# Optimization experiments

Measured on AMD Instinct MI355X. Metric: run time of the kernel, lower is better.

Reference implementation:

```python
import jax, jax.numpy as jnp
import numpy as np

D_MODEL, N_STATE, L_MAX, BATCH = 512, 64, 2048, 8


def _make_dplr_hippo(n):
    # HiPPO-LegS -> NPLR -> DPLR (Annotated-S4 construction)
    p0 = np.sqrt(1.0 + 2.0 * np.arange(n))
    A = p0[:, None] * p0[None, :]
    A = -(np.tril(A) - np.diag(np.arange(n)))
    p = np.sqrt(np.arange(n) + 0.5)
    S = A + p[:, None] * p[None, :]          # normal part (skew-symmetric + const diag)
    lam_re = np.mean(np.diagonal(S)) * np.ones(n)
    lam_im, V = np.linalg.eigh(S * (-1j))
    p_rot = V.conj().T @ p
    return (lam_re.astype(np.float32), lam_im.astype(np.float32),
            p_rot.real.astype(np.float32), p_rot.imag.astype(np.float32))


def setup_inputs() -> dict:
    key = jax.random.key(0)
    k = jax.random.split(key, 8)
    lam_re, lam_im, p_re, p_im = _make_dplr_hippo(N_STATE)
    dt_min, dt_max = 1e-3, 1e-1
    log_step = (jax.random.uniform(k[0], (D_MODEL,))
                * (np.log(dt_max) - np.log(dt_min)) + np.log(dt_min)).astype(jnp.float32)
    s = 0.5 ** 0.5
    B_re = jax.random.normal(k[1], (D_MODEL, N_STATE), dtype=jnp.float32) * s
    B_im = jax.random.normal(k[2], (D_MODEL, N_STATE), dtype=jnp.float32) * s
    Ct_re = jax.random.normal(k[3], (D_MODEL, N_STATE), dtype=jnp.float32) * s
    Ct_im = jax.random.normal(k[4], (D_MODEL, N_STATE), dtype=jnp.float32) * s
    D = jnp.ones((D_MODEL,), jnp.float32)
    lim = 1.0 / np.sqrt(D_MODEL)
    W = jax.random.uniform(k[5], (D_MODEL, D_MODEL), minval=-lim, maxval=lim, dtype=jnp.float32)
    b = jax.random.uniform(k[6], (D_MODEL,), minval=-lim, maxval=lim, dtype=jnp.float32)
    u = jax.random.normal(k[7], (BATCH, L_MAX, D_MODEL), dtype=jnp.float32)
    return dict(u=u,
                lam_re=jnp.asarray(lam_re), lam_im=jnp.asarray(lam_im),
                p_re=jnp.asarray(p_re), p_im=jnp.asarray(p_im),
                B_re=B_re, B_im=B_im, Ct_re=Ct_re, Ct_im=Ct_im,
                log_step=log_step, D=D, W=W, b=b,
                ln_w=jnp.ones((D_MODEL,), jnp.float32),
                ln_b=jnp.zeros((D_MODEL,), jnp.float32))


def _s4_kernel(lam, p, Bc, Ct, step, L):
    # lam, p: (n,) complex; Bc, Ct: (H, n) complex; step: (H,)
    omega = jnp.exp((-2j * jnp.pi) * (jnp.arange(L) / L))          # (L,) roots of unity
    g = (2.0 / step[:, None]) * ((1.0 - omega) / (1.0 + omega))    # (H, L) bilinear transform
    c = 2.0 / (1.0 + omega)                                        # (L,)
    cauchy = 1.0 / (g[:, :, None] - lam)                           # (H, L, n)
    a0, a1 = Ct.conj(), jnp.conj(p)[None, :]
    b0, b1 = Bc, p[None, :]
    k00 = jnp.einsum('hn,hln->hl', a0 * b0, cauchy)
    k01 = jnp.einsum('hn,hln->hl', a0 * b1, cauchy)
    k10 = jnp.einsum('hn,hln->hl', a1 * b0, cauchy)
    k11 = jnp.einsum('hn,hln->hl', a1 * b1, cauchy)
    at_roots = c * (k00 - k01 * (1.0 / (1.0 + k11)) * k10)         # generating fn at roots
    return jnp.fft.ifft(at_roots, n=L, axis=-1).real               # (H, L) real SSM kernel


def reference(u, lam_re, lam_im, p_re, p_im, B_re, B_im, Ct_re, Ct_im,
              log_step, D, W, b, ln_w, ln_b):
    L = u.shape[1]
    lam = lam_re + 1j * lam_im
    p = p_re + 1j * p_im
    Bc = B_re + 1j * B_im
    Ct = Ct_re + 1j * Ct_im
    K = _s4_kernel(lam, p, Bc, Ct, jnp.exp(log_step), L)           # (H, L)
    # causal (non-circular) convolution via zero-padded FFT
    nfft = 2 * L
    Kf = jnp.fft.rfft(K, n=nfft, axis=-1)                          # (H, L+1)
    Uf = jnp.fft.rfft(u, n=nfft, axis=1)                           # (B, L+1, H)
    y = jnp.fft.irfft(Uf * Kf.T[None], n=nfft, axis=1)[:, :L]      # (B, L, H)
    y = y + D * u                                                  # skip connection
    z = jax.nn.gelu(y, approximate=False)                          # GELU (dropout p=0)
    z = jnp.einsum('blh,oh->blo', z, W) + b                        # Linear(d_model, d_model)
    r = z + u                                                      # residual
    mean = r.mean(-1, keepdims=True)
    var = r.var(-1, keepdims=True)
    return (r - mean) / jnp.sqrt(var + 1e-5) * ln_w + ln_b         # LayerNorm
```

## Files before the change

kernel.cpp:

```cpp
#include <hip/hip_runtime.h>
#include <hip/hip_bf16.h>
#include <math.h>

#define PI_F 3.14159265358979f

typedef __attribute__((ext_vector_type(8))) short bf16x8;
typedef __attribute__((ext_vector_type(4))) float f32x4;
typedef __attribute__((ext_vector_type(2))) float f32x2;

#define DM 512
#define LSEQ 2048
#define NB 8
#define NFFT 4096
#define MTOK (NB*LSEQ)

__device__ __forceinline__ float frcp(float x) { return __builtin_amdgcn_rcpf(x); }

__device__ __forceinline__ float gelu_fast(float y) {
  float t = 0.79788456f * (y + 0.044715f * y * y * y);
  float e = __expf(2.0f * t);
  float th = 1.0f - 2.0f * frcp(e + 1.0f);
  return 0.5f * y * (1.0f + th);
}

__device__ __forceinline__ int PD(int i) { return i + (i >> 5); }
#define LDSN 4224

template<bool INV>
__device__ __forceinline__ void dft8(const float xr[8], const float xi[8],
                                     float yr[8], float yi[8]) {
  const float C = 0.70710678118654752f;
  float t0r=xr[0]+xr[4], t0i=xi[0]+xi[4];
  float t1r=xr[0]-xr[4], t1i=xi[0]-xi[4];
  float t2r=xr[2]+xr[6], t2i=xi[2]+xi[6];
  float t3r=xr[2]-xr[6], t3i=xi[2]-xi[6];
  float it3r = INV ? -t3i : t3i;
  float it3i = INV ?  t3r : -t3r;
  float E0r=t0r+t2r, E0i=t0i+t2i;
  float E2r=t0r-t2r, E2i=t0i-t2i;
  float E1r=t1r+it3r, E1i=t1i+it3i;
  float E3r=t1r-it3r, E3i=t1i-it3i;
  float u0r=xr[1]+xr[5], u0i=xi[1]+xi[5];
  float u1r=xr[1]-xr[5], u1i=xi[1]-xi[5];
  float u2r=xr[3]+xr[7], u2i=xi[3]+xi[7];
  float u3r=xr[3]-xr[7], u3i=xi[3]-xi[7];
  float iu3r = INV ? -u3i : u3i;
  float iu3i = INV ?  u3r : -u3r;
  float O0r=u0r+u2r, O0i=u0i+u2i;
  float O2r=u0r-u2r, O2i=u0i-u2i;
  float O1r=u1r+iu3r, O1i=u1i+iu3i;
  float O3r=u1r-iu3r, O3i=u1i-iu3i;
  float w1r = INV ? C*(O1r-O1i) : C*(O1r+O1i);
  float w1i = INV ? C*(O1r+O1i) : C*(O1i-O1r);
  float w2r = INV ? -O2i : O2i;
  float w2i = INV ?  O2r : -O2r;
  float w3r = INV ? -C*(O3r+O3i) : C*(O3i-O3r);
  float w3i = INV ?  C*(O3r-O3i) : -C*(O3r+O3i);
  yr[0]=E0r+O0r; yi[0]=E0i+O0i;
  yr[4]=E0r-O0r; yi[4]=E0i-O0i;
  yr[1]=E1r+w1r; yi[1]=E1i+w1i;
  yr[5]=E1r-w1r; yi[5]=E1i-w1i;
  yr[2]=E2r+w2r; yi[2]=E2i+w2i;
  yr[6]=E2r-w2r; yi[6]=E2i-w2i;
  yr[3]=E3r+w3r; yi[3]=E3i+w3i;
  yr[7]=E3r-w3r; yi[7]=E3i-w3i;
}

template<bool INV>
__device__ __forceinline__ void dft16(const float xr[16], const float xi[16],
                                      float yr[16], float yi[16]) {
  float exr[8], exi[8], oxr[8], oxi[8];
  #pragma unroll
  for (int m = 0; m < 8; ++m) {
    exr[m]=xr[2*m];   exi[m]=xi[2*m];
    oxr[m]=xr[2*m+1]; oxi[m]=xi[2*m+1];
  }
  float er[8], ei[8], orr[8], oii[8];
  dft8<INV>(exr, exi, er, ei);
  dft8<INV>(oxr, oxi, orr, oii);
  const float KC = 0.92387953251128675f;
  const float KS = 0.38268343236508977f;
  const float KH = 0.70710678118654752f;
  float tr, ti;
  yr[0]=er[0]+orr[0]; yi[0]=ei[0]+oii[0];
  yr[8]=er[0]-orr[0]; yi[8]=ei[0]-oii[0];
  { float a=KC, b=INV?KS:-KS;
    tr=orr[1]*a-oii[1]*b; ti=orr[1]*b+oii[1]*a;
    yr[1]=er[1]+tr; yi[1]=ei[1]+ti; yr[9]=er[1]-tr; yi[9]=ei[1]-ti; }
  { float a=KH, b=INV?KH:-KH;
    tr=orr[2]*a-oii[2]*b; ti=orr[2]*b+oii[2]*a;
    yr[2]=er[2]+tr; yi[2]=ei[2]+ti; yr[10]=er[2]-tr; yi[10]=ei[2]-ti; }
  { float a=KS, b=INV?KC:-KC;
    tr=orr[3]*a-oii[3]*b; ti=orr[3]*b+oii[3]*a;
    yr[3]=er[3]+tr; yi[3]=ei[3]+ti; yr[11]=er[3]-tr; yi[11]=ei[3]-ti; }
  { if (INV) { tr=-oii[4]; ti= orr[4]; } else { tr= oii[4]; ti=-orr[4]; }
    yr[4]=er[4]+tr; yi[4]=ei[4]+ti; yr[12]=er[4]-tr; yi[12]=ei[4]-ti; }
  { float a=-KS, b=INV?KC:-KC;
    tr=orr[5]*a-oii[5]*b; ti=orr[5]*b+oii[5]*a;
    yr[5]=er[5]+tr; yi[5]=ei[5]+ti; yr[13]=er[5]-tr; yi[13]=ei[5]-ti; }
  { float a=-KH, b=INV?KH:-KH;
    tr=orr[6]*a-oii[6]*b; ti=orr[6]*b+oii[6]*a;
    yr[6]=er[6]+tr; yi[6]=ei[6]+ti; yr[14]=er[6]-tr; yi[14]=ei[6]-ti; }
  { float a=-KC, b=INV?KS:-KS;
    tr=orr[7]*a-oii[7]*b; ti=orr[7]*b+oii[7]*a;
    yr[7]=er[7]+tr; yi[7]=ei[7]+ti; yr[15]=er[7]-tr; yi[15]=ei[7]-ti; }
}

template<bool INV, int NSLOG, int NBF>
__device__ __forceinline__ void r16s(float* sr, float* si, int tid,
                                     float c1, float s1f) {
  float yr[16], yi[16];
  bool act = (NBF >= 256) || (tid < NBF);
  __syncthreads();
  if (act) {
    float xr[16], xi[16];
    #pragma unroll
    for (int m = 0; m < 16; ++m) {
      int ix = PD(tid + m * NBF);
      xr[m] = sr[ix]; xi[m] = si[ix];
    }
    if (NSLOG > 0) {
      float s1 = INV ? -s1f : s1f;
      float wr = c1, wi = s1;
      #pragma unroll
      for (int m = 1; m < 16; ++m) {
        float tr = xr[m]*wr - xi[m]*wi;
        float ti = xr[m]*wi + xi[m]*wr;
        xr[m] = tr; xi[m] = ti;
        float nr = wr*c1 - wi*s1;
        float ni = wr*s1 + wi*c1;
        wr = nr; wi = ni;
      }
    }
    dft16<INV>(xr, xi, yr, yi);
  }
  __syncthreads();
  if (act) {
    int r = tid & ((1 << NSLOG) - 1);
    int q = tid >> NSLOG;
    int base = (q << (NSLOG + 4)) + r;
    #pragma unroll
    for (int p = 0; p < 16; ++p) {
      int ix = PD(base + (p << NSLOG));
      sr[ix] = yr[p]; si[ix] = yi[p];
    }
  }
}

__device__ __forceinline__ void r16s_zfirst(float* sr, float* si, int tid) {
  const float KC = 0.92387953251128675f;
  const float KS = 0.38268343236508977f;
  const float KH = 0.70710678118654752f;
  float xr[8], xi[8];
  __syncthreads();
  #pragma unroll
  for (int m = 0; m < 8; ++m) {
    int ix = PD(tid + m * 256);
    xr[m] = sr[ix]; xi[m] = si[ix];
  }
  float er[8], ei[8];
  dft8<false>(xr, xi, er, ei);
  float tr[8], ti[8];
  tr[0] = xr[0];                      ti[0] = xi[0];
  tr[1] =  xr[1]*KC + xi[1]*KS;       ti[1] =  xi[1]*KC - xr[1]*KS;
  tr[2] = (xr[2] + xi[2])*KH;         ti[2] = (xi[2] - xr[2])*KH;
  tr[3] =  xr[3]*KS + xi[3]*KC;       ti[3] =  xi[3]*KS - xr[3]*KC;
  tr[4] =  xi[4];                     ti[4] = -xr[4];
  tr[5] = -xr[5]*KS + xi[5]*KC;       ti[5] = -xi[5]*KS - xr[5]*KC;
  tr[6] = (xi[6] - xr[6])*KH;         ti[6] = -(xr[6] + xi[6])*KH;
  tr[7] = -xr[7]*KC + xi[7]*KS;       ti[7] = -xi[7]*KC - xr[7]*KS;
  float odr[8], odi[8];
  dft8<false>(tr, ti, odr, odi);
  __syncthreads();
  int base = tid << 4;
  #pragma unroll
  for (int j = 0; j < 8; ++j) {
    int ie = PD(base + 2*j), io = PD(base + 2*j + 1);
    sr[ie] = er[j];  si[ie] = ei[j];
    sr[io] = odr[j]; si[io] = odi[j];
  }
}

template<bool INV, int NSLOG, int NBF>
__device__ __forceinline__ void r8s(float* sr, float* si, int tid,
                                    float c1, float s1f) {
  float yr[8], yi[8];
  bool act = (NBF >= 256) || (tid < NBF);
  __syncthreads();
  if (act) {
    float xr[8], xi[8];
    #pragma unroll
    for (int m = 0; m < 8; ++m) {
      int ix = PD(tid + m * NBF);
      xr[m] = sr[ix]; xi[m] = si[ix];
    }
    if (NSLOG > 0) {
      float s1 = INV ? -s1f : s1f;
      float wr = c1, wi = s1;
      #pragma unroll
      for (int m = 1; m < 8; ++m) {
        float tr = xr[m]*wr - xi[m]*wi;
        float ti = xr[m]*wi + xi[m]*wr;
        xr[m] = tr; xi[m] = ti;
        float nr = wr*c1 - wi*s1;
        float ni = wr*s1 + wi*c1;
        wr = nr; wi = ni;
      }
    }
    dft8<INV>(xr, xi, yr, yi);
  }
  __syncthreads();
  if (act) {
    int r = tid & ((1 << NSLOG) - 1);
    int q = tid >> NSLOG;
    int base = (q << (NSLOG + 3)) + r;
    #pragma unroll
    for (int p = 0; p < 8; ++p) {
      int ix = PD(base + (p << NSLOG));
      sr[ix] = yr[p]; si[ix] = yi[p];
    }
  }
}

template<bool INV>
__device__ __forceinline__ void fft4096(float* sr, float* si, int tid,
                                        float cA, float sA, float cB, float sB) {
  r16s<INV, 0, 256>(sr, si, tid, 1.f, 0.f);
  r16s<INV, 4, 256>(sr, si, tid, cA, sA);
  r16s<INV, 8, 256>(sr, si, tid, cB, sB);
  __syncthreads();
}

__device__ __forceinline__ void fft4096z(float* sr, float* si, int tid,
                                         float cA, float sA, float cB, float sB) {
  r16s_zfirst(sr, si, tid);
  r16s<false, 4, 256>(sr, si, tid, cA, sA);
  r16s<false, 8, 256>(sr, si, tid, cB, sB);
  __syncthreads();
}

template<bool INV>
__device__ __forceinline__ void fft2048(float* sr, float* si, int tid,
                                        float cA, float sA, float cB, float sB) {
  r8s <INV, 0, 256>(sr, si, tid, 1.f, 0.f);
  r16s<INV, 3, 128>(sr, si, tid, cA, sA);
  r16s<INV, 7, 128>(sr, si, tid, cB, sB);
  __syncthreads();
}

__global__ __launch_bounds__(256) void k_prep(
    const float* __restrict__ lam_re, const float* __restrict__ lam_im,
    const float* __restrict__ p_re,   const float* __restrict__ p_im,
    const float* __restrict__ B_re,   const float* __restrict__ B_im,
    const float* __restrict__ Ct_re,  const float* __restrict__ Ct_im,
    float* __restrict__ wtab, float4* __restrict__ otab) {
  int bidx = blockIdx.x;
  if (bidx < 128) {
    int idx = bidx * 256 + threadIdx.x;
    int n = idx & 63;
    float br = B_re[idx],  bi = B_im[idx];
    float cr = Ct_re[idx], ci = Ct_im[idx];
    float pr = p_re[n],    pi = p_im[n];
    float* w = wtab + (size_t)idx * 12;
    w[0] = cr*br + ci*bi;   w[1] = cr*bi - ci*br;
    w[2] = cr*pr + ci*pi;   w[3] = cr*pi - ci*pr;
    w[4] = pr*br + pi*bi;   w[5] = pr*bi - pi*br;
    w[6] = pr*pr + pi*pi;   w[7] = lam_re[n];
    w[8] = lam_im[n];       w[9] = 0.f; w[10] = 0.f; w[11] = 0.f;
  } else {
    int l = (bidx - 128) * 256 + threadIdx.x;
    float omi, omr;
    sincosf(-2.0f * PI_F * (float)l / (float)LSEQ, &omi, &omr);
    float a = 1.0f + omr;
    float iv = frcp(a*a + omi*omi);
    float4 o;
    o.x = 2.0f * a * iv;
    o.y = -2.0f * omi * iv;
    o.z = (1.0f - omr*omr - omi*omi) * iv;
    o.w = (-2.0f * omi) * iv;
    otab[l] = o;
  }
}

__global__ __launch_bounds__(256) void k_mega(
    const float* __restrict__ wtab, const float4* __restrict__ otab,
    const float* __restrict__ log_step, float2* __restrict__ atr,
    const float* __restrict__ u, float* __restrict__ ut,
    const float* __restrict__ W, __hip_bfloat16* __restrict__ Wb) {
  __shared__ float tsh[32][33];
  int bidx = blockIdx.x;
  int tid = threadIdx.x;
  int x = tid & 31, y0 = tid >> 5;

  float ur[4][4];
  #pragma unroll
  for (int t = 0; t < 4; ++t) {
    int id = bidx*4 + t;
    int lx = id & 63, hy = (id >> 6) & 15, b = id >> 10;
    int l0 = lx*32, h0 = hy*32;
    #pragma unroll
    for (int i = 0; i < 4; ++i) {
      int y = y0 + i*8;
      ur[t][i] = u[((size_t)b*LSEQ + l0 + y)*DM + h0 + x];
    }
  }
  bool doW = bidx < 1024;
  int wi = bidx*256 + tid;
  float wv = doW ? W[wi] : 0.0f;

  {
    int h = bidx >> 2;
    int l0 = ((bidx & 3) << 8) + tid;
    int l1 = l0 + 1024;
    float tos = 2.0f * expf(-log_step[h]);
    float4 o0 = otab[l0];
    float4 o1 = otab[l1];
    float cr0 = o0.x, ci0 = o0.y, cr1 = o1.x, ci1 = o1.y;
    f32x2 gr, gi;
    gr.x = tos * o0.z;  gr.y = tos * o1.z;
    gi.x = tos * o0.w;  gi.y = tos * o1.w;
    f32x2 K00r={0.f,0.f},K00i={0.f,0.f},K01r={0.f,0.f},K01i={0.f,0.f},
          K10r={0.f,0.f},K10i={0.f,0.f},K11r={0.f,0.f},K11i={0.f,0.f};
    const float4* wq = (const float4*)(wtab + (size_t)h * 64 * 12);
    #pragma unroll 8
    for (int n = 0; n < 64; ++n) {
      float4 wa = wq[n*3+0];
      float4 wb = wq[n*3+1];
      float  lim = wq[n*3+2].x;
      f32x2 dr = gr - wb.w;
      f32x2 di = gi - lim;
      f32x2 den = dr*dr + di*di;
      float ip = frcp(den.x * den.y);
      f32x2 inv; inv.x = den.y * ip; inv.y = den.x * ip;
      f32x2 car = dr*inv, cai = -di*inv;
      K00r += wa.x*car - wa.y*cai;  K00i += wa.x*cai + wa.y*car;
      K01r += wa.z*car - wa.w*cai;  K01i += wa.z*cai + wa.w*car;
      K10r += wb.x*car - wb.y*cai;  K10i += wb.x*cai + wb.y*car;
      K11r += wb.z*car;             K11i += wb.z*cai;
    }
    {
      float tr = K01r.x*K10r.x - K01i.x*K10i.x, ti = K01r.x*K10i.x + K01i.x*K10r.x;
      float d1r = 1.0f + K11r.x, d1i = K11i.x;
      float invd1 = frcp(d1r*d1r + d1i*d1i);
      float t2r = (tr*d1r + ti*d1i) * invd1;
      float t2i = (ti*d1r - tr*d1i) * invd1;
      float numr = K00r.x - t2r, numi = K00i.x - t2i;
      atr[(size_t)h * LSEQ + l0] = make_float2(cr0*numr - ci0*numi, cr0*numi + ci0*numr);
    }
    {
      float tr = K01r.y*K10r.y - K01i.y*K10i.y, ti = K01r.y*K10i.y + K01i.y*K10r.y;
      float d1r = 1.0f + K11r.y, d1i = K11i.y;
      float invd1 = frcp(d1r*d1r + d1i*d1i);
      float t2r = (tr*d1r + ti*d1i) * invd1;
      float t2i = (ti*d1r - tr*d1i) * invd1;
      float numr = K00r.y - t2r, numi = K00i.y - t2i;
      atr[(size_t)h * LSEQ + l1] = make_float2(cr1*numr - ci1*numi, cr1*numi + ci1*numr);
    }
  }

  if (doW) Wb[wi] = __float2bfloat16(wv);
  #pragma unroll
  for (int t = 0; t < 4; ++t) {
    int id = bidx*4 + t;
    int lx = id & 63, hy = (id >> 6) & 15, b = id >> 10;
    int l0 = lx*32, h0 = hy*32;
    __syncthreads();
    #pragma unroll
    for (int i = 0; i < 4; ++i)
      tsh[y0 + i*8][x] = ur[t][i];
    __syncthreads();
    #pragma unroll
    for (int i = 0; i < 4; ++i) {
      int y = y0 + i*8;
      ut[((size_t)b*DM + h0 + y)*LSEQ + l0 + x] = tsh[x][y];
    }
  }
}

__global__ __launch_bounds__(256, 4) void k_fftK(const float2* __restrict__ atr,
                                                 float2* __restrict__ Kf) {
  __shared__ float sr[LDSN], si[LDSN];
  int h = blockIdx.x, tid = threadIdx.x;
  float c2a, s2a, c2b, s2b, c4a, s4a, c4b, s4b;
  { int r = tid & 7;   __sincosf(-2.f*PI_F*(float)r/128.f,  &s2a, &c2a); }
  { int r = tid & 127; __sincosf(-2.f*PI_F*(float)r/2048.f, &s2b, &c2b); }
  { int r = tid & 15;  __sincosf(-2.f*PI_F*(float)r/256.f,  &s4a, &c4a); }
  { int r = tid;       __sincosf(-2.f*PI_F*(float)r/4096.f, &s4b, &c4b); }
  const float2* ap = atr + (size_t)h * LSEQ;
  #pragma unroll
  for (int i = 0; i < 8; ++i) {
    int l = tid + i*256;
    float2 v = ap[l];
    sr[PD(l)] = v.x; si[PD(l)] = v.y;
  }
  fft2048<true>(sr, si, tid, c2a, s2a, c2b, s2b);
  #pragma unroll
  for (int i = 0; i < 8; ++i) {
    int m = tid + i*256;
    float v = sr[PD(m)] * (1.0f / (float)LSEQ);
    sr[PD(m)] = v;
    si[PD(m)] = 0.0f;
  }
  fft4096z(sr, si, tid, c4a, s4a, c4b, s4b);
  float2* ko = Kf + (size_t)h * NFFT;
  #pragma unroll
  for (int i = 0; i < 16; ++i) {
    int f = tid + i*256;
    ko[f] = make_float2(sr[PD(f)], si[PD(f)]);
  }
}

__global__ __launch_bounds__(256, 4) void k_conv(const float* __restrict__ ut,
                                                 const float2* __restrict__ Kf,
                                                 const float* __restrict__ Dvec,
                                                 __hip_bfloat16* __restrict__ zbt) {
  __shared__ float sr[LDSN], si[LDSN];
  int wg = blockIdx.x;
  int bp = wg >> 9, h = wg & 511;
  int b0 = bp*2, b1 = bp*2 + 1;
  int tid = threadIdx.x;
  float c4a, s4a, c4b, s4b;
  { int r = tid & 15; __sincosf(-2.f*PI_F*(float)r/256.f,  &s4a, &c4a); }
  { int r = tid;      __sincosf(-2.f*PI_F*(float)r/4096.f, &s4b, &c4b); }
  const float* u0p = ut + ((size_t)(b0*DM + h)) * LSEQ;
  const float* u1p = ut + ((size_t)(b1*DM + h)) * LSEQ;
  #pragma unroll
  for (int i = 0; i < 8; ++i) {
    int l = tid + i*256;
    sr[PD(l)] = u0p[l];  si[PD(l)] = u1p[l];
  }
  fft4096z(sr, si, tid, c4a, s4a, c4b, s4b);
  float yrg[16], yig[16];
  const float2* kp = Kf + (size_t)h * NFFT;
  #pragma unroll
  for (int i = 0; i < 16; ++i) {
    int f = tid + i*256;
    int fn = (NFFT - f) & (NFFT - 1);
    float ar = sr[PD(f)],  ai = si[PD(f)];
    float br = sr[PD(fn)], bi = -si[PD(fn)];
    float u0r = 0.5f*(ar + br), u0i = 0.5f*(ai + bi);
    float u1r = 0.5f*(ai - bi), u1i = -0.5f*(ar - br);
    float2 K0 = kp[f];
    float y0r = u0r*K0.x - u0i*K0.y, y0i = u0r*K0.y + u0i*K0.x;
    float y1r = u1r*K0.x - u1i*K0.y, y1i = u1r*K0.y + u1i*K0.x;
    yrg[i] = y0r - y1i;
    yig[i] = y0i + y1r;
  }
  __syncthreads();
  #pragma unroll
  for (int i = 0; i < 16; ++i) {
    int f = tid + i*256;
    sr[PD(f)] = yrg[i]; si[PD(f)] = yig[i];
  }
  fft4096<true>(sr, si, tid, c4a, s4a, c4b, s4b);
  float d = Dvec[h];
  __hip_bfloat16* zb0 = zbt + ((size_t)(b0*DM + h)) * LSEQ;
  __hip_bfloat16* zb1 = zbt + ((size_t)(b1*DM + h)) * LSEQ;
  const float inv_n = 1.0f / (float)NFFT;
  #pragma unroll
  for (int i = 0; i < 8; ++i) {
    int l = tid + i*256;
    float y0 = sr[PD(l)]*inv_n + d*u0p[l];
    float y1 = si[PD(l)]*inv_n + d*u1p[l];
    zb0[l] = __float2bfloat16(gelu_fast(y0));
    zb1[l] = __float2bfloat16(gelu_fast(y1));
  }
}

__global__ __launch_bounds__(512) void k_gemm_ln(
    const ushort* __restrict__ zbt,
    const short* __restrict__ Wb,
    const float* __restrict__ bias,
    const float* __restrict__ u,
    const float* __restrict__ lnw, const float* __restrict__ lnb,
    float* __restrict__ out) {
  __shared__ ushort sA[64][40];
  __shared__ short sB[512][40];
  __shared__ float red[2][4][64];
  __shared__ float smu[64], srs[64];
  __shared__ float sln[2][DM];
  int tid = threadIdx.x, wave = tid >> 6, lane = tid & 63;
  int wm = wave >> 2, wn = wave & 3;
  int m0 = blockIdx.x * 64;
  int b = m0 >> 11;
  int l0 = m0 & (LSEQ - 1);
  const ushort* zb = zbt + (size_t)b * DM * LSEQ;
  int row = lane & 15, kq8 = (lane >> 4) << 3;
  int kk = tid >> 4, seg = tid & 15;
  int cB = (tid & 3) << 3, rB = tid >> 2;
  sln[0][tid] = lnw[tid];
  sln[1][tid] = lnb[tid];
  f32x4 acc[2][8];
  #pragma unroll
  for (int i = 0; i < 2; ++i)
    #pragma unroll
    for (int j = 0; j < 8; ++j) acc[i][j] = (f32x4){0.f,0.f,0.f,0.f};
  for (int k0 = 0; k0 < DM; k0 += 32) {
    __syncthreads();
    {
      uint2 v = *(const uint2*)(zb + (size_t)(k0 + kk)*LSEQ + l0 + seg*4);
      const ushort* p = (const ushort*)&v;
      sA[seg*4 + 0][kk] = p[0];
      sA[seg*4 + 1][kk] = p[1];
      sA[seg*4 + 2][kk] = p[2];
      sA[seg*4 + 3][kk] = p[3];
    }
    #pragma unroll
    for (int jj = 0; jj < 4; ++jj) {
      int o = rB + jj*128;
      *(uint4*)&sB[o][cB] = *(const uint4*)(Wb + (size_t)o*DM + k0 + cB);
    }
    __syncthreads();
    bf16x8 a0 = *(const bf16x8*)&sA[wm*32 + row][kq8];
    bf16x8 a1 = *(const bf16x8*)&sA[wm*32 + 16 + row][kq8];
    #pragma unroll
    for (int nt = 0; nt < 8; ++nt) {
      bf16x8 bf = *(const bf16x8*)&sB[wn*128 + nt*16 + row][kq8];
      acc[0][nt] = __builtin_amdgcn_mfma_f32_16x16x32_bf16(a0, bf, acc[0][nt], 0, 0, 0);
      acc[1][nt] = __builtin_amdgcn_mfma_f32_16x16x32_bf16(a1, bf, acc[1][nt], 0, 0, 0);
    }
  }
  int ccol = lane & 15, crow = (lane >> 4) << 2;
  #pragma unroll
  for (int rt = 0; rt < 2; ++rt) {
    #pragma unroll
    for (int rr = 0; rr < 4; ++rr) {
      int lr = wm*32 + rt*16 + crow + rr;
      int gr = m0 + lr;
      float ls = 0.f, ls2 = 0.f;
      #pragma unroll
      for (int nt = 0; nt < 8; ++nt) {
        int col = wn*128 + nt*16 + ccol;
        float v = acc[rt][nt][rr] + bias[col] + u[(size_t)gr*DM + col];
        acc[rt][nt][rr] = v;
        ls += v; ls2 += v*v;
      }
      ls  += __shfl_xor(ls, 1);  ls2 += __shfl_xor(ls2, 1);
      ls  += __shfl_xor(ls, 2);  ls2 += __shfl_xor(ls2, 2);
      ls  += __shfl_xor(ls, 4);  ls2 += __shfl_xor(ls2, 4);
      ls  += __shfl_xor(ls, 8);  ls2 += __shfl_xor(ls2, 8);
      if (ccol == 0) { red[0][wn][lr] = ls; red[1][wn][lr] = ls2; }
    }
  }
  __syncthreads();
  if (tid < 64) {
    float s = red[0][0][tid] + red[0][1][tid] + red[0][2][tid] + red[0][3][tid];
    float q = red[1][0][tid] + red[1][1][tid] + red[1][2][tid] + red[1][3][tid];
    float mean = s * (1.0f/(float)DM);
    float var  = q * (1.0f/(float)DM) - mean*mean;
    smu[tid] = mean;
    srs[tid] = rsqrtf(var + 1e-5f);
  }
  __syncthreads();
  #pragma unroll
  for (int rt = 0; rt < 2; ++rt) {
    #pragma unroll
    for (int rr = 0; rr < 4; ++rr) {
      int lr = wm*32 + rt*16 + crow + rr;
      int gr = m0 + lr;
      float mu = smu[lr], rs = srs[lr];
      #pragma unroll
      for (int nt = 0; nt < 8; ++nt) {
        int col = wn*128 + nt*16 + ccol;
        out[(size_t)gr*DM + col] = (acc[rt][nt][rr] - mu) * rs * sln[0][col] + sln[1][col];
      }
    }
  }
}

extern "C" void kernel_launch(void* const* d_in, const int* in_sizes, int n_in,
                              void* d_out, int out_size, void* d_ws, size_t ws_size,
                              hipStream_t stream) {
  const float* u        = (const float*)d_in[0];
  const float* lam_re   = (const float*)d_in[1];
  const float* lam_im   = (const float*)d_in[2];
  const float* p_re     = (const float*)d_in[3];
  const float* p_im     = (const float*)d_in[4];
  const float* B_re     = (const float*)d_in[5];
  const float* B_im     = (const float*)d_in[6];
  const float* Ct_re    = (const float*)d_in[7];
  const float* Ct_im    = (const float*)d_in[8];
  const float* log_step = (const float*)d_in[9];
  const float* Dv       = (const float*)d_in[10];
  const float* W        = (const float*)d_in[11];
  const float* bias     = (const float*)d_in[12];
  const float* ln_w     = (const float*)d_in[13];
  const float* ln_b     = (const float*)d_in[14];
  float* out = (float*)d_out;
  char* ws = (char*)d_ws;

  float2* Kf = (float2*)ws;
  float*  ut = (float*)(ws + (16u << 20));
  __hip_bfloat16* zbt = (__hip_bfloat16*)(ws + (48u << 20));
  float2* atr  = (float2*)(ws + (48u << 20));
  float*  wtab = (float*)(ws + (56u << 20));
  float4* otab = (float4*)(ws + (58u << 20));
  __hip_bfloat16* Wb = (__hip_bfloat16*)(ws + (64u << 20));
  if (ws_size < (65u << 20)) return;

  k_prep<<<dim3(136), dim3(256), 0, stream>>>(lam_re, lam_im, p_re, p_im,
                                              B_re, B_im, Ct_re, Ct_im, wtab, otab);
  k_mega<<<dim3(2048), dim3(256), 0, stream>>>(
      wtab, otab, log_step, atr, u, ut, W, Wb);
  k_fftK<<<dim3(DM), dim3(256), 0, stream>>>(atr, Kf);
  k_conv<<<dim3((NB/2) * DM), dim3(256), 0, stream>>>(ut, Kf, Dv, zbt);
  k_gemm_ln<<<dim3(MTOK/64), dim3(512), 0, stream>>>((const ushort*)zbt, (const short*)Wb,
                                                     bias, u, ln_w, ln_b, out);
}
```

Baseline: 127.8 us.

## Fuse Cauchy kernel evaluation, u transpose and W cast into the K FFT kernel

Merges the Cauchy/DPLR kernel-generation kernel and the per-channel FFT kernel into one per-channel block. The block keeps the generated spectrum in registers and writes it into LDS for the FFT, so the atr intermediate no longer goes through global memory and one launch is removed. It also absorbs the u transpose and the W bf16 cast. The cost is a grid that shrinks from 2048 blocks to 512, and each thread now holds 64 prefetched u values plus 8 spectrum values, which raises register pressure and may cut occupancy.

```diff
diff --git a/kernel.cpp b/kernel.cpp
--- a/kernel.cpp
+++ b/kernel.cpp
@@ -282,20 +282,19 @@
   }
 }
 
-__global__ __launch_bounds__(256) void k_mega(
+__global__ __launch_bounds__(256) void k_cfft(
     const float* __restrict__ wtab, const float4* __restrict__ otab,
-    const float* __restrict__ log_step, float2* __restrict__ atr,
+    const float* __restrict__ log_step, float2* __restrict__ Kf,
     const float* __restrict__ u, float* __restrict__ ut,
     const float* __restrict__ W, __hip_bfloat16* __restrict__ Wb) {
-  __shared__ float tsh[32][33];
-  int bidx = blockIdx.x;
-  int tid = threadIdx.x;
+  __shared__ float sr[LDSN], si[LDSN];
+  int h = blockIdx.x, tid = threadIdx.x;
   int x = tid & 31, y0 = tid >> 5;
 
-  float ur[4][4];
-  #pragma unroll
-  for (int t = 0; t < 4; ++t) {
-    int id = bidx*4 + t;
+  float ur[16][4];
+  #pragma unroll
+  for (int t = 0; t < 16; ++t) {
+    int id = h*16 + t;
     int lx = id & 63, hy = (id >> 6) & 15, b = id >> 10;
     int l0 = lx*32, h0 = hy*32;
     #pragma unroll
@@ -304,94 +303,104 @@
       ur[t][i] = u[((size_t)b*LSEQ + l0 + y)*DM + h0 + x];
     }
   }
-  bool doW = bidx < 1024;
-  int wi = bidx*256 + tid;
-  float wv = doW ? W[wi] : 0.0f;
-
-  {
-    int h = bidx >> 2;
-    int l0 = ((bidx & 3) << 8) + tid;
-    int l1 = l0 + 1024;
-    float tos = 2.0f * expf(-log_step[h]);
-    float4 o0 = otab[l0];
-    float4 o1 = otab[l1];
-    float cr0 = o0.x, ci0 = o0.y, cr1 = o1.x, ci1 = o1.y;
-    f32x2 gr, gi;
-    gr.x = tos * o0.z;  gr.y = tos * o1.z;
-    gi.x = tos * o0.w;  gi.y = tos * o1.w;
-    f32x2 K00r={0.f,0.f},K00i={0.f,0.f},K01r={0.f,0.f},K01i={0.f,0.f},
-          K10r={0.f,0.f},K10i={0.f,0.f},K11r={0.f,0.f},K11i={0.f,0.f};
-    const float4* wq = (const float4*)(wtab + (size_t)h * 64 * 12);
-    #pragma unroll 8
-    for (int n = 0; n < 64; ++n) {
-      float4 wa = wq[n*3+0];
-      float4 wb = wq[n*3+1];
-      float  lim = wq[n*3+2].x;
-      f32x2 dr = gr - wb.w;
-      f32x2 di = gi - lim;
-      f32x2 den = dr*dr + di*di;
-      float ip = frcp(den.x * den.y);
-      f32x2 inv; inv.x = den.y * ip; inv.y = den.x * ip;
-      f32x2 car = dr*inv, cai = -di*inv;
-      K00r += wa.x*car - wa.y*cai;  K00i += wa.x*cai + wa.y*car;
-      K01r += wa.z*car - wa.w*cai;  K01i += wa.z*cai + wa.w*car;
-      K10r += wb.x*car - wb.y*cai;  K10i += wb.x*cai + wb.y*car;
-      K11r += wb.z*car;             K11i += wb.z*cai;
-    }
-    {
-      float tr = K01r.x*K10r.x - K01i.x*K10i.x, ti = K01r.x*K10i.x + K01i.x*K10r.x;
-      float d1r = 1.0f + K11r.x, d1i = K11i.x;
-      float invd1 = frcp(d1r*d1r + d1i*d1i);
-      float t2r = (tr*d1r + ti*d1i) * invd1;
-      float t2i = (ti*d1r - tr*d1i) * invd1;
-      float numr = K00r.x - t2r, numi = K00i.x - t2i;
-      atr[(size_t)h * LSEQ + l0] = make_float2(cr0*numr - ci0*numi, cr0*numi + ci0*numr);
-    }
-    {
-      float tr = K01r.y*K10r.y - K01i.y*K10i.y, ti = K01r.y*K10i.y + K01i.y*K10r.y;
-      float d1r = 1.0f + K11r.y, d1i = K11i.y;
-      float invd1 = frcp(d1r*d1r + d1i*d1i);
-      float t2r = (tr*d1r + ti*d1i) * invd1;
-      float t2i = (ti*d1r - tr*d1i) * invd1;
-      float numr = K00r.y - t2r, numi = K00i.y - t2i;
-      atr[(size_t)h * LSEQ + l1] = make_float2(cr1*numr - ci1*numi, cr1*numi + ci1*numr);
-    }
-  }
-
-  if (doW) Wb[wi] = __float2bfloat16(wv);
-  #pragma unroll
-  for (int t = 0; t < 4; ++t) {
-    int id = bidx*4 + t;
-    int lx = id & 63, hy = (id >> 6) & 15, b = id >> 10;
-    int l0 = lx*32, h0 = hy*32;
-    __syncthreads();
-    #pragma unroll
-    for (int i = 0; i < 4; ++i)
-      tsh[y0 + i*8][x] = ur[t][i];
-    __syncthreads();
-    #pragma unroll
-    for (int i = 0; i < 4; ++i) {
-      int y = y0 + i*8;
-      ut[((size_t)b*DM + h0 + y)*LSEQ + l0 + x] = tsh[x][y];
-    }
-  }
-}
-
-__global__ __launch_bounds__(256, 4) void k_fftK(const float2* __restrict__ atr,
-                                                 float2* __restrict__ Kf) {
-  __shared__ float sr[LDSN], si[LDSN];
-  int h = blockIdx.x, tid = threadIdx.x;
+  int wi0 = h*512 + tid, wi1 = wi0 + 256;
+  float wv0 = W[wi0], wv1 = W[wi1];
+
   float c2a, s2a, c2b, s2b, c4a, s4a, c4b, s4b;
   { int r = tid & 7;   __sincosf(-2.f*PI_F*(float)r/128.f,  &s2a, &c2a); }
   { int r = tid & 127; __sincosf(-2.f*PI_F*(float)r/2048.f, &s2b, &c2b); }
   { int r = tid & 15;  __sincosf(-2.f*PI_F*(float)r/256.f,  &s4a, &c4a); }
   { int r = tid;       __sincosf(-2.f*PI_F*(float)r/4096.f, &s4b, &c4b); }
-  const float2* ap = atr + (size_t)h * LSEQ;
-  #pragma unroll
-  for (int i = 0; i < 8; ++i) {
-    int l = tid + i*256;
-    float2 v = ap[l];
-    sr[PD(l)] = v.x; si[PD(l)] = v.y;
+
+  float atre[8], atim[8];
+  float tos = 2.0f * expf(-log_step[h]);
+  const float4* wq = (const float4*)(wtab + (size_t)h * 64 * 12);
+  #pragma unroll
+  for (int gq = 0; gq < 2; ++gq) {
+    int la = tid + (gq*2 + 0)*256;
+    int lb = tid + (gq*2 + 1)*256;
+    float4 oa0 = otab[la], oa1 = otab[la + 1024];
+    float4 ob0 = otab[lb], ob1 = otab[lb + 1024];
+    f32x2 grA, giA, grB, giB;
+    grA.x = tos*oa0.z; grA.y = tos*oa1.z; giA.x = tos*oa0.w; giA.y = tos*oa1.w;
+    grB.x = tos*ob0.z; grB.y = tos*ob1.z; giB.x = tos*ob0.w; giB.y = tos*ob1.w;
+    f32x2 A00r={0,0},A00i={0,0},A01r={0,0},A01i={0,0},
+          A10r={0,0},A10i={0,0},A11r={0,0},A11i={0,0};
+    f32x2 B00r={0,0},B00i={0,0},B01r={0,0},B01i={0,0},
+          B10r={0,0},B10i={0,0},B11r={0,0},B11i={0,0};
+    #pragma unroll 4
+    for (int n = 0; n < 64; ++n) {
+      float4 wa = wq[n*3+0];
+      float4 wb = wq[n*3+1];
+      float  lim = wq[n*3+2].x;
+      { f32x2 dr = grA - wb.w, di = giA - lim;
+        f32x2 den = dr*dr + di*di;
+        float ip = frcp(den.x * den.y);
+        f32x2 inv; inv.x = den.y * ip; inv.y = den.x * ip;
+        f32x2 car = dr*inv, cai = -di*inv;
+        A00r += wa.x*car - wa.y*cai;  A00i += wa.x*cai + wa.y*car;
+        A01r += wa.z*car - wa.w*cai;  A01i += wa.z*cai + wa.w*car;
+        A10r += wb.x*car - wb.y*cai;  A10i += wb.x*cai + wb.y*car;
+        A11r += wb.z*car;             A11i += wb.z*cai; }
+      { f32x2 dr = grB - wb.w, di = giB - lim;
+        f32x2 den = dr*dr + di*di;
+        float ip = frcp(den.x * den.y);
+        f32x2 inv; inv.x = den.y * ip; inv.y = den.x * ip;
+        f32x2 car = dr*inv, cai = -di*inv;
+        B00r += wa.x*car - wa.y*cai;  B00i += wa.x*cai + wa.y*car;
+        B01r += wa.z*car - wa.w*cai;  B01i += wa.z*cai + wa.w*car;
+        B10r += wb.x*car - wb.y*cai;  B10i += wb.x*cai + wb.y*car;
+        B11r += wb.z*car;             B11i += wb.z*cai; }
+    }
+    #pragma unroll
+    for (int s = 0; s < 4; ++s) {
+      float K00r = (s==0)?A00r.x:(s==1)?A00r.y:(s==2)?B00r.x:B00r.y;
+      float K00i = (s==0)?A00i.x:(s==1)?A00i.y:(s==2)?B00i.x:B00i.y;
+      float K01r = (s==0)?A01r.x:(s==1)?A01r.y:(s==2)?B01r.x:B01r.y;
+      float K01i = (s==0)?A01i.x:(s==1)?A01i.y:(s==2)?B01i.x:B01i.y;
+      float K10r = (s==0)?A10r.x:(s==1)?A10r.y:(s==2)?B10r.x:B10r.y;
+      float K10i = (s==0)?A10i.x:(s==1)?A10i.y:(s==2)?B10i.x:B10i.y;
+      float K11r = (s==0)?A11r.x:(s==1)?A11r.y:(s==2)?B11r.x:B11r.y;
+      float K11i = (s==0)?A11i.x:(s==1)?A11i.y:(s==2)?B11i.x:B11i.y;
+      float4 oo = (s==0)?oa0:(s==1)?oa1:(s==2)?ob0:ob1;
+      float tr = K01r*K10r - K01i*K10i, ti = K01r*K10i + K01i*K10r;
+      float d1r = 1.0f + K11r, d1i = K11i;
+      float invd1 = frcp(d1r*d1r + d1i*d1i);
+      float t2r = (tr*d1r + ti*d1i) * invd1;
+      float t2i = (ti*d1r - tr*d1i) * invd1;
+      float numr = K00r - t2r, numi = K00i - t2i;
+      int slot = gq*2 + (s>>1) + (s&1)*4;
+      atre[slot] = oo.x*numr - oo.y*numi;
+      atim[slot] = oo.x*numi + oo.y*numr;
+    }
+  }
+
+  Wb[wi0] = __float2bfloat16(wv0);
+  Wb[wi1] = __float2bfloat16(wv1);
+  float (*tsh)[33] = (float(*)[33])sr;
+  #pragma unroll
+  for (int t = 0; t < 16; ++t) {
+    int id = h*16 + t;
+    int lx = id & 63, hy = (id >> 6) & 15, b = id >> 10;
+    int l0 = lx*32, h0 = hy*32;
+    __syncthreads();
+    #pragma unroll
+    for (int i = 0; i < 4; ++i)
+      tsh[y0 + i*8][x] = ur[t][i];
+    __syncthreads();
+    #pragma unroll
+    for (int i = 0; i < 4; ++i) {
+      int y = y0 + i*8;
+      ut[((size_t)b*DM + h0 + y)*LSEQ + l0 + x] = tsh[x][y];
+    }
+  }
+
+  __syncthreads();
+  #pragma unroll
+  for (int j = 0; j < 4; ++j) {
+    int l = tid + j*256;
+    sr[PD(l)] = atre[j];          si[PD(l)] = atim[j];
+    sr[PD(l + 1024)] = atre[j+4]; si[PD(l + 1024)] = atim[j+4];
   }
   fft2048<true>(sr, si, tid, c2a, s2a, c2b, s2b);
   #pragma unroll
@@ -592,7 +601,6 @@
   float2* Kf = (float2*)ws;
   float*  ut = (float*)(ws + (16u << 20));
   __hip_bfloat16* zbt = (__hip_bfloat16*)(ws + (48u << 20));
-  float2* atr  = (float2*)(ws + (48u << 20));
   float*  wtab = (float*)(ws + (56u << 20));
   float4* otab = (float4*)(ws + (58u << 20));
   __hip_bfloat16* Wb = (__hip_bfloat16*)(ws + (64u << 20));
@@ -600,9 +608,8 @@
 
   k_prep<<<dim3(136), dim3(256), 0, stream>>>(lam_re, lam_im, p_re, p_im,
                                               B_re, B_im, Ct_re, Ct_im, wtab, otab);
-  k_mega<<<dim3(2048), dim3(256), 0, stream>>>(
-      wtab, otab, log_step, atr, u, ut, W, Wb);
-  k_fftK<<<dim3(DM), dim3(256), 0, stream>>>(atr, Kf);
+  k_cfft<<<dim3(DM), dim3(256), 0, stream>>>(wtab, otab, log_step, Kf,
+                                             u, ut, W, Wb);
   k_conv<<<dim3((NB/2) * DM), dim3(256), 0, stream>>>(ut, Kf, Dv, zbt);
   k_gemm_ln<<<dim3(MTOK/64), dim3(512), 0, stream>>>((const ushort*)zbt, (const short*)Wb,
                                                      bias, u, ln_w, ln_b, out);
```

After: 130.5 us. 1.02x slower.
